# Kernel optimization log

Measured on AMD Instinct MI355X. Metric: run time of the kernel, lower is better.

Reference implementation:

```python
import jax, jax.numpy as jnp
import numpy as np
import math

HEADS = 16
HEAD_DIM = 64
MODEL_DIM = HEADS * HEAD_DIM
SEQ = 2048
BATCH = 2


def setup_inputs() -> dict:
    key = jax.random.key(0)
    ks = jax.random.split(key, 11)
    s = 0.02
    return {
        "query": jax.random.normal(ks[0], (SEQ, BATCH, MODEL_DIM), jnp.float32),
        "key": jax.random.normal(ks[1], (SEQ, BATCH, MODEL_DIM), jnp.float32),
        "value": jax.random.normal(ks[2], (SEQ, BATCH, MODEL_DIM), jnp.float32),
        "mask": jnp.ones((1, SEQ, 1), jnp.int32),
        "Wq": jax.random.normal(ks[3], (MODEL_DIM, MODEL_DIM), jnp.float32) * s,
        "bq": jax.random.normal(ks[4], (MODEL_DIM,), jnp.float32) * s,
        "Wk": jax.random.normal(ks[5], (MODEL_DIM, MODEL_DIM), jnp.float32) * s,
        "bk": jax.random.normal(ks[6], (MODEL_DIM,), jnp.float32) * s,
        "Wv": jax.random.normal(ks[7], (MODEL_DIM, MODEL_DIM), jnp.float32) * s,
        "bv": jax.random.normal(ks[8], (MODEL_DIM,), jnp.float32) * s,
        "Wo": jax.random.normal(ks[9], (MODEL_DIM, MODEL_DIM), jnp.float32) * s,
        "bo": jax.random.normal(ks[10], (MODEL_DIM,), jnp.float32) * s,
    }


def _proj(x, W, b):
    # torch nn.Linear: y = x @ W.T + b ; then view to [.., H, D]
    y = jnp.einsum("sbm,nm->sbn", x, W) + b
    return y.reshape(x.shape[0], x.shape[1], HEADS, HEAD_DIM)


def reference(query, key, value, mask, Wq, bq, Wk, bk, Wv, bv, Wo, bo):
    # NOTE: original module applies mask to `score` AFTER softmax has been
    # taken, and the masked score is discarded -> mask has no effect.
    del mask
    seq_len, batch_size, _ = query.shape
    scale = 1.0 / math.sqrt(HEAD_DIM)
    q = _proj(query, Wq, bq)   # [S,B,H,D]
    k = _proj(key, Wk, bk)
    v = _proj(value, Wv, bv)
    score = jnp.einsum("ibhd,jbhd->ijbh", q, k) * scale  # [S,S,B,H]
    attn = jax.nn.softmax(score, axis=1)  # softmax over key axis j
    # dropout: eval-mode identity (deterministic baseline)
    x = jnp.einsum("ijbh,jbhd->ibhd", attn, v)
    x = x.reshape(seq_len, batch_size, MODEL_DIM)
    return jnp.einsum("sbm,nm->sbn", x, Wo) + bo
```

## Files before the change

kernel.cpp:

```cpp
#include <hip/hip_runtime.h>

#define SEQ    2048
#define NBATCH 2
#define NHEAD  16
#define HD     64
#define MD     1024
#define TOK    (SEQ * NBATCH)
#define WN8    (MD * MD / 8)

typedef __attribute__((ext_vector_type(4)))  float f32x4;
typedef __attribute__((ext_vector_type(16))) float f32x16;
typedef __attribute__((ext_vector_type(8)))  short bf16x8;
typedef __attribute__((ext_vector_type(8)))  unsigned short u16x8;

__device__ __forceinline__ unsigned short f2bf(float f) {
  union { float f; unsigned int u; } x; x.f = f;
  unsigned int u = x.u + 0x7fffu + ((x.u >> 16) & 1u);
  return (unsigned short)(u >> 16);
}

__device__ __forceinline__ unsigned cvtpk(float lo, float hi) {
  unsigned r;
  asm("v_cvt_pk_bf16_f32 %0, %1, %2" : "=v"(r) : "v"(lo), "v"(hi));
  return r;
}
__device__ __forceinline__ void plswap(unsigned &a, unsigned &b) {
  asm volatile("v_permlane32_swap_b32 %0, %1" : "+v"(a), "+v"(b));
}

__device__ __forceinline__ void gload_lds16(const void* g, void* l) {
  typedef const __attribute__((address_space(1))) unsigned int* gp_t;
  typedef __attribute__((address_space(3))) unsigned int* lp_t;
  __builtin_amdgcn_global_load_lds((gp_t)g, (lp_t)l, 16, 0, 0);
}

__global__ __launch_bounds__(256) void cvt_w(
    const float* __restrict__ wq, const float* __restrict__ wk,
    const float* __restrict__ wv, const float* __restrict__ wo,
    unsigned short* __restrict__ owq, unsigned short* __restrict__ owk,
    unsigned short* __restrict__ owv, unsigned short* __restrict__ owo) {
  const int i = blockIdx.x * 256 + threadIdx.x;
  const int s = i >> 17;
  const int r = i & (WN8 - 1);
  const float* src = s == 0 ? wq : (s == 1 ? wk : (s == 2 ? wv : wo));
  unsigned short* dst = s == 0 ? owq : (s == 1 ? owk : (s == 2 ? owv : owo));
  const float4* p = (const float4*)src + (size_t)r * 2;
  float4 a = p[0];
  float4 b = p[1];
  u16x8 o;
  o[0] = f2bf(a.x); o[1] = f2bf(a.y); o[2] = f2bf(a.z); o[3] = f2bf(a.w);
  o[4] = f2bf(b.x); o[5] = f2bf(b.y); o[6] = f2bf(b.z); o[7] = f2bf(b.w);
  *((u16x8*)dst + r) = o;
}

__global__ __launch_bounds__(512) void gemm_qkv(
    const float* __restrict__ Xq, const float* __restrict__ Xk,
    const float* __restrict__ Xv, const unsigned short* __restrict__ Wq,
    const unsigned short* __restrict__ Wk, const unsigned short* __restrict__ Wv,
    const float* __restrict__ bq, const float* __restrict__ bk, const float* __restrict__ bv,
    unsigned short* __restrict__ Qo, unsigned short* __restrict__ Ko,
    unsigned short* __restrict__ Vo, float qscale) {
  __shared__ unsigned short sA[3][128 * 32];
  __shared__ unsigned short sB[3][128 * 32];
  const int tid  = threadIdx.x;
  const int lane = tid & 63;
  const int wave = tid >> 6;
  const int wm   = (wave >> 2) << 6;
  const int wn   = (wave & 3) << 5;
  const int l15  = lane & 15;
  const int g    = lane >> 4;

  const int flat = blockIdx.x + (blockIdx.y << 3) + (blockIdx.z << 8);
  const int nx   = (flat & 63) >> 3;
  const int gr   = ((flat >> 6) << 3) + (flat & 7);
  const int ny   = gr & 31;
  const int z    = gr >> 5;

  const float* Xf; const unsigned short* Wb; const float* bias;
  if (z == 0)      { Xf = Xq; Wb = Wq; bias = bq; }
  else if (z == 1) { Xf = Xk; Wb = Wk; bias = bk; }
  else             { Xf = Xv; Wb = Wv; bias = bv; }
  int bM, bN;
  if (z < 2) { bM = ny << 7; bN = nx << 7; }
  else       { bM = nx << 7; bN = ny << 7; }
  const int bX = (z < 2) ? bM : bN;
  const int bW = (z < 2) ? bN : bM;
  unsigned short* sX3 = (z < 2) ? &sA[0][0] : &sB[0][0];
  unsigned short* sW3 = (z < 2) ? &sB[0][0] : &sA[0][0];

  f32x4 acc[4][2];
#pragma unroll
  for (int a_ = 0; a_ < 4; ++a_)
#pragma unroll
    for (int b_ = 0; b_ < 2; ++b_)
      acc[a_][b_] = f32x4{0.f, 0.f, 0.f, 0.f};

  const int r = tid >> 2, cc = tid & 3;
  const float* xsrc = Xf + (size_t)(bX + r) * MD + cc * 8;
  const unsigned short* wsrc = Wb + (size_t)(bW + r) * MD + cc * 8;

  float4 ra0, rb0, ra1, rb1;
  auto xissue0 = [&](int kt) {
    ra0 = *(const float4*)(xsrc + (kt << 5));
    rb0 = *(const float4*)(xsrc + (kt << 5) + 4);
  };
  auto xissue1 = [&](int kt) {
    ra1 = *(const float4*)(xsrc + (kt << 5));
    rb1 = *(const float4*)(xsrc + (kt << 5) + 4);
  };
  auto xwrite0 = [&](int c) {
    union { unsigned u[4]; bf16x8 v; } w;
    w.u[0] = cvtpk(ra0.x, ra0.y); w.u[1] = cvtpk(ra0.z, ra0.w);
    w.u[2] = cvtpk(rb0.x, rb0.y); w.u[3] = cvtpk(rb0.z, rb0.w);
    *(bf16x8*)(sX3 + c * 4096 + tid * 8) = w.v;
  };
  auto xwrite1 = [&](int c) {
    union { unsigned u[4]; bf16x8 v; } w;
    w.u[0] = cvtpk(ra1.x, ra1.y); w.u[1] = cvtpk(ra1.z, ra1.w);
    w.u[2] = cvtpk(rb1.x, rb1.y); w.u[3] = cvtpk(rb1.z, rb1.w);
    *(bf16x8*)(sX3 + c * 4096 + tid * 8) = w.v;
  };
  auto wissue = [&](int c, int kt) {
    gload_lds16(wsrc + (kt << 5), (char*)(sW3 + c * 4096) + tid * 16);
  };

  auto mfma_step = [&](int c) {
    bf16x8 af[4], bfr[2];
#pragma unroll
    for (int f = 0; f < 4; ++f)
      af[f] = *(const bf16x8*)&sA[c][(wm + f * 16 + l15) * 32 + g * 8];
#pragma unroll
    for (int f = 0; f < 2; ++f)
      bfr[f] = *(const bf16x8*)&sB[c][(wn + f * 16 + l15) * 32 + g * 8];
#pragma unroll
    for (int mf = 0; mf < 4; ++mf)
#pragma unroll
      for (int nf = 0; nf < 2; ++nf)
        acc[mf][nf] = __builtin_amdgcn_mfma_f32_16x16x32_bf16(af[mf], bfr[nf], acc[mf][nf], 0, 0, 0);
  };

  const int nk = MD >> 5;
  auto endwait = [&](int e) {
    if (e + 4 < nk)      asm volatile("s_waitcnt vmcnt(3)" ::: "memory");
    else if (e + 2 < nk) asm volatile("s_waitcnt vmcnt(1)" ::: "memory");
    else                 asm volatile("s_waitcnt vmcnt(0)" ::: "memory");
    asm volatile("s_waitcnt lgkmcnt(0)" ::: "memory");
    __builtin_amdgcn_s_barrier();
  };

  xissue0(0);
  xissue1(1);
  wissue(0, 0);
  wissue(1, 1);
  asm volatile("s_waitcnt vmcnt(4)" ::: "memory");
  xwrite0(0);
  asm volatile("s_waitcnt vmcnt(2)" ::: "memory");
  xwrite1(1);
  xissue0(2);
  xissue1(3);
  asm volatile("s_waitcnt vmcnt(4)" ::: "memory");
  asm volatile("s_waitcnt lgkmcnt(0)" ::: "memory");
  __builtin_amdgcn_s_barrier();

  for (int kt = 0; kt < nk; kt += 2) {
    if (kt + 2 < nk) { xwrite0((kt + 2) % 3); wissue((kt + 2) % 3, kt + 2); }
    if (kt + 4 < nk) xissue0(kt + 4);
    mfma_step(kt % 3);
    endwait(kt);
    if (kt + 3 < nk) { xwrite1((kt + 3) % 3); wissue((kt + 3) % 3, kt + 3); }
    if (kt + 5 < nk) xissue1(kt + 5);
    mfma_step((kt + 1) % 3);
    if (kt + 2 < nk) endwait(kt + 1);
  }

  if (z < 2) {
    unsigned short* O = (z == 0) ? Qo : Ko;
    const float scale = (z == 0) ? qscale : 1.0f;
#pragma unroll
    for (int nf = 0; nf < 2; ++nf) {
      const int cch = bN + wn + nf * 16 + l15;
      const float bb = bias[cch];
      const int h = cch >> 6, d = cch & 63;
#pragma unroll
      for (int mf = 0; mf < 4; ++mf)
#pragma unroll
        for (int i = 0; i < 4; ++i) {
          const int t = bM + wm + mf * 16 + (g << 2) + i;
          const int b = t & 1, s = t >> 1;
          O[((((b << 4) + h) * SEQ + s) << 6) + d] = f2bf((acc[mf][nf][i] + bb) * scale);
        }
    }
  } else {
#pragma unroll
    for (int mf = 0; mf < 4; ++mf)
#pragma unroll
      for (int i = 0; i < 4; ++i) {
        const int rch = bM + wm + mf * 16 + (g << 2) + i;
        const float bb = bias[rch];
        const int h = rch >> 6, d = rch & 63;
#pragma unroll
        for (int nf = 0; nf < 2; ++nf) {
          const int t = bN + wn + nf * 16 + l15;
          const int b = t & 1, s = t >> 1;
          Vo[((((b << 4) + h) << 6) + d) * SEQ + s] = f2bf(acc[mf][nf][i] + bb);
        }
      }
  }
}

__global__ __launch_bounds__(1024) void gemm_oproj(const unsigned short* __restrict__ A,
                                                   const unsigned short* __restrict__ B,
                                                   const float* __restrict__ bias,
                                                   float* __restrict__ O) {
  __shared__ unsigned short sA[3][128 * 32];
  __shared__ unsigned short sB[3][128 * 32];
  const int tid  = threadIdx.x;
  const int lane = tid & 63;
  const int wave = tid >> 6;
  const int wm   = (wave >> 2) << 5;
  const int wn   = (wave & 3) << 5;
  const int l15  = lane & 15;
  const int g    = lane >> 4;

  const int flat = blockIdx.x + (blockIdx.y << 3);
  const int nx   = (flat & 63) >> 3;
  const int gr   = ((flat >> 6) << 3) + (flat & 7);
  const int bM   = gr << 7;
  const int bN   = nx << 7;

  f32x4 acc[2][2];
#pragma unroll
  for (int a_ = 0; a_ < 2; ++a_)
#pragma unroll
    for (int b_ = 0; b_ < 2; ++b_)
      acc[a_][b_] = f32x4{0.f, 0.f, 0.f, 0.f};

  const int ct = tid & 511;
  const int r = ct >> 2, cc = ct & 3;
  const unsigned short* srow = (tid < 512)
      ? A + (size_t)(bM + r) * MD + cc * 8
      : B + (size_t)(bN + r) * MD + cc * 8;
  unsigned short* sdst3 = (tid < 512) ? &sA[0][0] : &sB[0][0];
  auto stage = [&](int c, int kt) {
    gload_lds16(srow + (kt << 5), (char*)(sdst3 + c * 4096) + ct * 16);
  };

  const int nk = MD >> 5;
  stage(0, 0);
  stage(1, 1);
  asm volatile("s_waitcnt vmcnt(1)" ::: "memory");
  __builtin_amdgcn_s_barrier();

  int cur = 0;
  for (int kt = 0; kt < nk; ++kt) {
    if (kt + 2 < nk) stage(cur == 0 ? 2 : cur - 1, kt + 2);
    bf16x8 af[2], bfr[2];
#pragma unroll
    for (int f = 0; f < 2; ++f)
      af[f] = *(const bf16x8*)&sA[cur][(wm + f * 16 + l15) * 32 + g * 8];
#pragma unroll
    for (int f = 0; f < 2; ++f)
      bfr[f] = *(const bf16x8*)&sB[cur][(wn + f * 16 + l15) * 32 + g * 8];
#pragma unroll
    for (int mf = 0; mf < 2; ++mf)
#pragma unroll
      for (int nf = 0; nf < 2; ++nf)
        acc[mf][nf] = __builtin_amdgcn_mfma_f32_16x16x32_bf16(af[mf], bfr[nf], acc[mf][nf], 0, 0, 0);
    if (kt + 2 < nk)
      asm volatile("s_waitcnt vmcnt(1)" ::: "memory");
    else if (kt + 1 < nk)
      asm volatile("s_waitcnt vmcnt(0)" ::: "memory");
    if (kt + 1 < nk) __builtin_amdgcn_s_barrier();
    cur = (cur == 2) ? 0 : cur + 1;
  }

#pragma unroll
  for (int nf = 0; nf < 2; ++nf) {
    const int cch = bN + wn + nf * 16 + l15;
    const float bb = bias[cch];
#pragma unroll
    for (int mf = 0; mf < 2; ++mf)
#pragma unroll
      for (int i = 0; i < 4; ++i) {
        const int t = bM + wm + mf * 16 + (g << 2) + i;
        O[(size_t)t * MD + cch] = acc[mf][nf][i] + bb;
      }
  }
}

__global__ __launch_bounds__(512) void attn_fwd(const unsigned short* __restrict__ Qg,
                                                const unsigned short* __restrict__ Kg,
                                                const unsigned short* __restrict__ Vg,
                                                unsigned short* __restrict__ Xout) {
  __shared__ __align__(16) char smem[65536];
  char* sKc = smem;
  char* sVc = smem + 32768;

  const int tid  = threadIdx.x;
  const int lane = tid & 63;
  const int wave = tid >> 6;
  const int ws   = wave & 3;
  const int grp  = wave >> 2;
  const int l31  = lane & 31;
  const int half = lane >> 5;
  const int bh   = blockIdx.y;
  const int q0w  = (blockIdx.x << 7) + (ws << 5);

  const unsigned short* Qb = Qg + (size_t)bh * (SEQ * HD);
  const char* Kb = (const char*)(Kg + (size_t)bh * (SEQ * HD));
  const char* Vb = (const char*)(Vg + (size_t)bh * (HD * SEQ));

  bf16x8 qf[4];
#pragma unroll
  for (int c = 0; c < 4; ++c)
    qf[c] = *(const bf16x8*)&Qb[(size_t)(q0w + l31) * HD + c * 16 + half * 8];

  f32x16 acc_o[2];
#pragma unroll
  for (int dt = 0; dt < 2; ++dt)
#pragma unroll
    for (int e = 0; e < 16; ++e) acc_o[dt][e] = 0.f;
  float lrow = 0.f;

  auto stage = [&](int c, int kt) {
#pragma unroll
    for (int h = 0; h < 2; ++h) {
      const int p = tid << 4;
      const int row = p >> 7;
      const int lcol = (p ^ ((row & 7) << 4)) & 127;
      const int kbase = (h << 10) + (kt << 6);
      gload_lds16(Kb + (size_t)(kbase + row) * (HD * 2) + lcol,
                  sKc + ((h * 2 + c) << 13) + p);
      gload_lds16(Vb + (size_t)row * (SEQ * 2) + (kbase << 1) + lcol,
                  sVc + ((h * 2 + c) << 13) + p);
    }
  };

  const char* myK = sKc + (grp << 14);
  const char* myV = sVc + (grp << 14);

  stage(0, 0);
  __syncthreads();
  int cur = 0;

  const int NT = SEQ / 2 / 64;
  for (int kt = 0; kt < NT; ++kt) {
    if (kt + 1 < NT) stage(cur ^ 1, kt + 1);

    f32x16 accs[2];
    __builtin_amdgcn_s_setprio(1);
#pragma unroll
    for (int ks = 0; ks < 2; ++ks) {
#pragma unroll
      for (int e = 0; e < 16; ++e) accs[ks][e] = 0.f;
      const int krow = ks * 32 + l31;
      const int swz  = (krow & 7) << 4;
#pragma unroll
      for (int c = 0; c < 4; ++c) {
        const int off = (krow << 7) + ((c * 32 + half * 16) ^ swz);
        bf16x8 kf = *(const bf16x8*)(myK + ((cur) << 13) + off);
        accs[ks] = __builtin_amdgcn_mfma_f32_32x32x16_bf16(kf, qf[c], accs[ks], 0, 0, 0);
      }
    }
    __builtin_amdgcn_s_setprio(0);

    float rsum = 0.f;
#pragma unroll
    for (int ks = 0; ks < 2; ++ks)
#pragma unroll
      for (int e = 0; e < 16; ++e) {
        const float pv = __builtin_amdgcn_exp2f(accs[ks][e]);
        accs[ks][e] = pv;
        rsum += pv;
      }
    lrow += rsum;

    bf16x8 pa[4];
#pragma unroll
    for (int ks = 0; ks < 2; ++ks)
#pragma unroll
      for (int hc = 0; hc < 2; ++hc) {
        const int b = hc * 8;
        unsigned X  = cvtpk(accs[ks][b + 0], accs[ks][b + 1]);
        unsigned X2 = cvtpk(accs[ks][b + 2], accs[ks][b + 3]);
        unsigned Y  = cvtpk(accs[ks][b + 4], accs[ks][b + 5]);
        unsigned Y2 = cvtpk(accs[ks][b + 6], accs[ks][b + 7]);
        plswap(X, Y);
        plswap(X2, Y2);
        union { unsigned u[4]; bf16x8 v; } w;
        w.u[0] = X; w.u[1] = X2; w.u[2] = Y; w.u[3] = Y2;
        pa[ks * 2 + hc] = w.v;
      }

    __builtin_amdgcn_s_setprio(1);
#pragma unroll
    for (int dt = 0; dt < 2; ++dt) {
      const int drow = dt * 32 + l31;
      const int swz  = (drow & 7) << 4;
#pragma unroll
      for (int kc = 0; kc < 4; ++kc) {
        const int off = (drow << 7) + ((kc * 32 + half * 16) ^ swz);
        bf16x8 vf = *(const bf16x8*)(myV + ((cur) << 13) + off);
        acc_o[dt] = __builtin_amdgcn_mfma_f32_32x32x16_bf16(vf, pa[kc], acc_o[dt], 0, 0, 0);
      }
    }
    __builtin_amdgcn_s_setprio(0);

    __syncthreads();
    cur ^= 1;
  }

  float lt = lrow + __shfl_xor(lrow, 32);
  float* dump  = (float*)smem;
  float* ldump = dump + 4 * 32 * 68;
  const int base = (ws * 32 + l31) * 68;

  if (grp == 1) {
#pragma unroll
    for (int dt = 0; dt < 2; ++dt)
#pragma unroll
      for (int r4 = 0; r4 < 4; ++r4) {
        const int d0 = dt * 32 + r4 * 8 + half * 4;
        const int e = r4 * 4;
        *(float2*)&dump[base + d0]     = float2{acc_o[dt][e + 0], acc_o[dt][e + 1]};
        *(float2*)&dump[base + d0 + 2] = float2{acc_o[dt][e + 2], acc_o[dt][e + 3]};
      }
    if (half == 0) ldump[ws * 32 + l31] = lt;
  }
  __syncthreads();
  if (grp == 0) {
    const float ltot = lt + ldump[ws * 32 + l31];
    const float inv = 1.f / ltot;
    const int b = bh >> 4, h = bh & 15;
    const int s = q0w + l31;
    const int t = s * NBATCH + b;
    unsigned short* Ot = Xout + (size_t)t * MD + (h << 6);
#pragma unroll
    for (int dt = 0; dt < 2; ++dt)
#pragma unroll
      for (int r4 = 0; r4 < 4; ++r4) {
        const int d0 = dt * 32 + r4 * 8 + half * 4;
        const int e = r4 * 4;
        float2 a0 = *(float2*)&dump[base + d0];
        float2 a1 = *(float2*)&dump[base + d0 + 2];
        uint2 w;
        w.x = cvtpk((acc_o[dt][e + 0] + a0.x) * inv, (acc_o[dt][e + 1] + a0.y) * inv);
        w.y = cvtpk((acc_o[dt][e + 2] + a1.x) * inv, (acc_o[dt][e + 3] + a1.y) * inv);
        *(uint2*)(Ot + d0) = w;
      }
  }
}

extern "C" void kernel_launch(void* const* d_in, const int* in_sizes, int n_in,
                              void* d_out, int out_size, void* d_ws, size_t ws_size,
                              hipStream_t stream) {
  const float* query = (const float*)d_in[0];
  const float* key   = (const float*)d_in[1];
  const float* value = (const float*)d_in[2];
  const float* Wq = (const float*)d_in[4];
  const float* bq = (const float*)d_in[5];
  const float* Wk = (const float*)d_in[6];
  const float* bk = (const float*)d_in[7];
  const float* Wv = (const float*)d_in[8];
  const float* bv = (const float*)d_in[9];
  const float* Wo = (const float*)d_in[10];
  const float* bo = (const float*)d_in[11];

  char* ws = (char*)d_ws;
  const size_t MB = 1024 * 1024;
  unsigned short* Xa  = (unsigned short*)(ws + 0 * MB);
  unsigned short* Wqb = (unsigned short*)(ws + 24 * MB);
  unsigned short* Wkb = (unsigned short*)(ws + 26 * MB);
  unsigned short* Wvb = (unsigned short*)(ws + 28 * MB);
  unsigned short* Wob = (unsigned short*)(ws + 30 * MB);
  unsigned short* Qb  = (unsigned short*)(ws + 32 * MB);
  unsigned short* Kb  = (unsigned short*)(ws + 40 * MB);
  unsigned short* Vb  = (unsigned short*)(ws + 48 * MB);

  cvt_w<<<4 * WN8 / 256, 256, 0, stream>>>(Wq, Wk, Wv, Wo, Wqb, Wkb, Wvb, Wob);

  const float kQScale = 0.125f * 1.44269504088896340736f;
  dim3 gQKV(MD / 128, TOK / 128, 3);
  gemm_qkv<<<gQKV, 512, 0, stream>>>(query, key, value, Wqb, Wkb, Wvb,
                                     bq, bk, bv, Qb, Kb, Vb, kQScale);

  dim3 gA(SEQ / 128, NBATCH * NHEAD);
  attn_fwd<<<gA, 512, 0, stream>>>(Qb, Kb, Vb, Xa);

  dim3 gO(MD / 128, TOK / 128);
  gemm_oproj<<<gO, 1024, 0, stream>>>(Xa, Wob, bo, (float*)d_out);
  (void)in_sizes; (void)n_in; (void)out_size; (void)ws_size;
}
```

Baseline: 107.9 us.

## Split QKV GEMM loads across 1024 threads with X and W wave groups

Doubles the QKV projection block to 1024 threads. The first 512 threads load and convert the fp32 activations and the other 512 issue the direct-to-LDS weight loads, so each half has its own wait counters. All 16 waves now do MFMA on a 32x32 sub-tile instead of 8 waves doing 64x32, which halves accumulators per thread and adds waves to hide latency. In exchange, each wave does less MFMA work per LDS fragment read, and barrier cost is spread over more waves.

```diff
diff --git a/kernel.cpp b/kernel.cpp
--- a/kernel.cpp
+++ b/kernel.cpp
@@ -53,7 +53,7 @@
   *((u16x8*)dst + r) = o;
 }
 
-__global__ __launch_bounds__(512) void gemm_qkv(
+__global__ __launch_bounds__(1024) void gemm_qkv(
     const float* __restrict__ Xq, const float* __restrict__ Xk,
     const float* __restrict__ Xv, const unsigned short* __restrict__ Wq,
     const unsigned short* __restrict__ Wk, const unsigned short* __restrict__ Wv,
@@ -65,10 +65,11 @@
   const int tid  = threadIdx.x;
   const int lane = tid & 63;
   const int wave = tid >> 6;
-  const int wm   = (wave >> 2) << 6;
+  const int wm   = (wave >> 2) << 5;
   const int wn   = (wave & 3) << 5;
   const int l15  = lane & 15;
   const int g    = lane >> 4;
+  const bool isX = tid < 512;
 
   const int flat = blockIdx.x + (blockIdx.y << 3) + (blockIdx.z << 8);
   const int nx   = (flat & 63) >> 3;
@@ -88,14 +89,15 @@
   unsigned short* sX3 = (z < 2) ? &sA[0][0] : &sB[0][0];
   unsigned short* sW3 = (z < 2) ? &sB[0][0] : &sA[0][0];
 
-  f32x4 acc[4][2];
-#pragma unroll
-  for (int a_ = 0; a_ < 4; ++a_)
+  f32x4 acc[2][2];
+#pragma unroll
+  for (int a_ = 0; a_ < 2; ++a_)
 #pragma unroll
     for (int b_ = 0; b_ < 2; ++b_)
       acc[a_][b_] = f32x4{0.f, 0.f, 0.f, 0.f};
 
-  const int r = tid >> 2, cc = tid & 3;
+  const int ct = tid & 511;
+  const int r = ct >> 2, cc = ct & 3;
   const float* xsrc = Xf + (size_t)(bX + r) * MD + cc * 8;
   const unsigned short* wsrc = Wb + (size_t)(bW + r) * MD + cc * 8;
 
@@ -112,28 +114,28 @@
     union { unsigned u[4]; bf16x8 v; } w;
     w.u[0] = cvtpk(ra0.x, ra0.y); w.u[1] = cvtpk(ra0.z, ra0.w);
     w.u[2] = cvtpk(rb0.x, rb0.y); w.u[3] = cvtpk(rb0.z, rb0.w);
-    *(bf16x8*)(sX3 + c * 4096 + tid * 8) = w.v;
+    *(bf16x8*)(sX3 + c * 4096 + ct * 8) = w.v;
   };
   auto xwrite1 = [&](int c) {
     union { unsigned u[4]; bf16x8 v; } w;
     w.u[0] = cvtpk(ra1.x, ra1.y); w.u[1] = cvtpk(ra1.z, ra1.w);
     w.u[2] = cvtpk(rb1.x, rb1.y); w.u[3] = cvtpk(rb1.z, rb1.w);
-    *(bf16x8*)(sX3 + c * 4096 + tid * 8) = w.v;
+    *(bf16x8*)(sX3 + c * 4096 + ct * 8) = w.v;
   };
   auto wissue = [&](int c, int kt) {
-    gload_lds16(wsrc + (kt << 5), (char*)(sW3 + c * 4096) + tid * 16);
+    gload_lds16(wsrc + (kt << 5), (char*)(sW3 + c * 4096) + ct * 16);
   };
 
   auto mfma_step = [&](int c) {
-    bf16x8 af[4], bfr[2];
-#pragma unroll
-    for (int f = 0; f < 4; ++f)
+    bf16x8 af[2], bfr[2];
+#pragma unroll
+    for (int f = 0; f < 2; ++f)
       af[f] = *(const bf16x8*)&sA[c][(wm + f * 16 + l15) * 32 + g * 8];
 #pragma unroll
     for (int f = 0; f < 2; ++f)
       bfr[f] = *(const bf16x8*)&sB[c][(wn + f * 16 + l15) * 32 + g * 8];
 #pragma unroll
-    for (int mf = 0; mf < 4; ++mf)
+    for (int mf = 0; mf < 2; ++mf)
 #pragma unroll
       for (int nf = 0; nf < 2; ++nf)
         acc[mf][nf] = __builtin_amdgcn_mfma_f32_16x16x32_bf16(af[mf], bfr[nf], acc[mf][nf], 0, 0, 0);
@@ -141,34 +143,49 @@
 
   const int nk = MD >> 5;
   auto endwait = [&](int e) {
-    if (e + 4 < nk)      asm volatile("s_waitcnt vmcnt(3)" ::: "memory");
-    else if (e + 2 < nk) asm volatile("s_waitcnt vmcnt(1)" ::: "memory");
-    else                 asm volatile("s_waitcnt vmcnt(0)" ::: "memory");
+    if (isX) {
+      if (e + 4 < nk) asm volatile("s_waitcnt vmcnt(2)" ::: "memory");
+      else            asm volatile("s_waitcnt vmcnt(0)" ::: "memory");
+      asm volatile("s_waitcnt lgkmcnt(0)" ::: "memory");
+    } else {
+      if (e + 2 < nk) asm volatile("s_waitcnt vmcnt(1)" ::: "memory");
+      else            asm volatile("s_waitcnt vmcnt(0)" ::: "memory");
+    }
+    __builtin_amdgcn_s_barrier();
+  };
+
+  if (isX) {
+    xissue0(0);
+    xissue1(1);
+    asm volatile("s_waitcnt vmcnt(2)" ::: "memory");
+    xwrite0(0);
+    asm volatile("s_waitcnt vmcnt(0)" ::: "memory");
+    xwrite1(1);
+    xissue0(2);
+    xissue1(3);
     asm volatile("s_waitcnt lgkmcnt(0)" ::: "memory");
-    __builtin_amdgcn_s_barrier();
-  };
-
-  xissue0(0);
-  xissue1(1);
-  wissue(0, 0);
-  wissue(1, 1);
-  asm volatile("s_waitcnt vmcnt(4)" ::: "memory");
-  xwrite0(0);
-  asm volatile("s_waitcnt vmcnt(2)" ::: "memory");
-  xwrite1(1);
-  xissue0(2);
-  xissue1(3);
-  asm volatile("s_waitcnt vmcnt(4)" ::: "memory");
-  asm volatile("s_waitcnt lgkmcnt(0)" ::: "memory");
+  } else {
+    wissue(0, 0);
+    wissue(1, 1);
+    asm volatile("s_waitcnt vmcnt(0)" ::: "memory");
+  }
   __builtin_amdgcn_s_barrier();
 
   for (int kt = 0; kt < nk; kt += 2) {
-    if (kt + 2 < nk) { xwrite0((kt + 2) % 3); wissue((kt + 2) % 3, kt + 2); }
-    if (kt + 4 < nk) xissue0(kt + 4);
+    if (isX) {
+      if (kt + 2 < nk) xwrite0((kt + 2) % 3);
+      if (kt + 4 < nk) xissue0(kt + 4);
+    } else {
+      if (kt + 2 < nk) wissue((kt + 2) % 3, kt + 2);
+    }
     mfma_step(kt % 3);
     endwait(kt);
-    if (kt + 3 < nk) { xwrite1((kt + 3) % 3); wissue((kt + 3) % 3, kt + 3); }
-    if (kt + 5 < nk) xissue1(kt + 5);
+    if (isX) {
+      if (kt + 3 < nk) xwrite1((kt + 3) % 3);
+      if (kt + 5 < nk) xissue1(kt + 5);
+    } else {
+      if (kt + 3 < nk) wissue((kt + 3) % 3, kt + 3);
+    }
     mfma_step((kt + 1) % 3);
     if (kt + 2 < nk) endwait(kt + 1);
   }
@@ -182,7 +199,7 @@
       const float bb = bias[cch];
       const int h = cch >> 6, d = cch & 63;
 #pragma unroll
-      for (int mf = 0; mf < 4; ++mf)
+      for (int mf = 0; mf < 2; ++mf)
 #pragma unroll
         for (int i = 0; i < 4; ++i) {
           const int t = bM + wm + mf * 16 + (g << 2) + i;
@@ -192,7 +209,7 @@
     }
   } else {
 #pragma unroll
-    for (int mf = 0; mf < 4; ++mf)
+    for (int mf = 0; mf < 2; ++mf)
 #pragma unroll
       for (int i = 0; i < 4; ++i) {
         const int rch = bM + wm + mf * 16 + (g << 2) + i;
@@ -481,8 +498,8 @@
 
   const float kQScale = 0.125f * 1.44269504088896340736f;
   dim3 gQKV(MD / 128, TOK / 128, 3);
-  gemm_qkv<<<gQKV, 512, 0, stream>>>(query, key, value, Wqb, Wkb, Wvb,
-                                     bq, bk, bv, Qb, Kb, Vb, kQScale);
+  gemm_qkv<<<gQKV, 1024, 0, stream>>>(query, key, value, Wqb, Wkb, Wvb,
+                                      bq, bk, bv, Qb, Kb, Vb, kQScale);
 
   dim3 gA(SEQ / 128, NBATCH * NHEAD);
   attn_fwd<<<gA, 512, 0, stream>>>(Qb, Kb, Vb, Xa);
```

New measurement: 111.9 us. 1.04x slower.

## Replace triple-buffered QKV GEMM pipeline with simple double buffering

Applied to the files above, without the earlier changes.

The QKV projection GEMM drops its three-stage LDS ring, which prefetched two K-tiles ahead, and uses a two-buffer scheme instead. Each iteration now loads only the next tile, converts X to bf16 into LDS after the MFMA step, then waits and synchronises with a barrier. This cuts shared memory per block from about 48KB to 32KB and simplifies the wait-count bookkeeping, which may help occupancy. In exchange, less global-load latency is hidden behind compute, and there is a full vmcnt(0) wait plus a barrier on every K step.

```diff
diff --git a/kernel.cpp b/kernel.cpp
--- a/kernel.cpp
+++ b/kernel.cpp
@@ -60,8 +60,8 @@
     const float* __restrict__ bq, const float* __restrict__ bk, const float* __restrict__ bv,
     unsigned short* __restrict__ Qo, unsigned short* __restrict__ Ko,
     unsigned short* __restrict__ Vo, float qscale) {
-  __shared__ unsigned short sA[3][128 * 32];
-  __shared__ unsigned short sB[3][128 * 32];
+  __shared__ unsigned short sA[2][128 * 32];
+  __shared__ unsigned short sB[2][128 * 32];
   const int tid  = threadIdx.x;
   const int lane = tid & 63;
   const int wave = tid >> 6;
@@ -85,8 +85,8 @@
   else       { bM = nx << 7; bN = ny << 7; }
   const int bX = (z < 2) ? bM : bN;
   const int bW = (z < 2) ? bN : bM;
-  unsigned short* sX3 = (z < 2) ? &sA[0][0] : &sB[0][0];
-  unsigned short* sW3 = (z < 2) ? &sB[0][0] : &sA[0][0];
+  unsigned short* sX2 = (z < 2) ? &sA[0][0] : &sB[0][0];
+  unsigned short* sW2 = (z < 2) ? &sB[0][0] : &sA[0][0];
 
   f32x4 acc[4][2];
 #pragma unroll
@@ -99,29 +99,19 @@
   const float* xsrc = Xf + (size_t)(bX + r) * MD + cc * 8;
   const unsigned short* wsrc = Wb + (size_t)(bW + r) * MD + cc * 8;
 
-  float4 ra0, rb0, ra1, rb1;
-  auto xissue0 = [&](int kt) {
-    ra0 = *(const float4*)(xsrc + (kt << 5));
-    rb0 = *(const float4*)(xsrc + (kt << 5) + 4);
-  };
-  auto xissue1 = [&](int kt) {
-    ra1 = *(const float4*)(xsrc + (kt << 5));
-    rb1 = *(const float4*)(xsrc + (kt << 5) + 4);
-  };
-  auto xwrite0 = [&](int c) {
+  float4 ra, rb;
+  auto xissue = [&](int kt) {
+    ra = *(const float4*)(xsrc + (kt << 5));
+    rb = *(const float4*)(xsrc + (kt << 5) + 4);
+  };
+  auto xwrite = [&](int c) {
     union { unsigned u[4]; bf16x8 v; } w;
-    w.u[0] = cvtpk(ra0.x, ra0.y); w.u[1] = cvtpk(ra0.z, ra0.w);
-    w.u[2] = cvtpk(rb0.x, rb0.y); w.u[3] = cvtpk(rb0.z, rb0.w);
-    *(bf16x8*)(sX3 + c * 4096 + tid * 8) = w.v;
-  };
-  auto xwrite1 = [&](int c) {
-    union { unsigned u[4]; bf16x8 v; } w;
-    w.u[0] = cvtpk(ra1.x, ra1.y); w.u[1] = cvtpk(ra1.z, ra1.w);
-    w.u[2] = cvtpk(rb1.x, rb1.y); w.u[3] = cvtpk(rb1.z, rb1.w);
-    *(bf16x8*)(sX3 + c * 4096 + tid * 8) = w.v;
+    w.u[0] = cvtpk(ra.x, ra.y); w.u[1] = cvtpk(ra.z, ra.w);
+    w.u[2] = cvtpk(rb.x, rb.y); w.u[3] = cvtpk(rb.z, rb.w);
+    *(bf16x8*)(sX2 + c * 4096 + tid * 8) = w.v;
   };
   auto wissue = [&](int c, int kt) {
-    gload_lds16(wsrc + (kt << 5), (char*)(sW3 + c * 4096) + tid * 16);
+    gload_lds16(wsrc + (kt << 5), (char*)(sW2 + c * 4096) + tid * 16);
   };
 
   auto mfma_step = [&](int c) {
@@ -140,37 +130,24 @@
   };
 
   const int nk = MD >> 5;
-  auto endwait = [&](int e) {
-    if (e + 4 < nk)      asm volatile("s_waitcnt vmcnt(3)" ::: "memory");
-    else if (e + 2 < nk) asm volatile("s_waitcnt vmcnt(1)" ::: "memory");
-    else                 asm volatile("s_waitcnt vmcnt(0)" ::: "memory");
-    asm volatile("s_waitcnt lgkmcnt(0)" ::: "memory");
-    __builtin_amdgcn_s_barrier();
-  };
-
-  xissue0(0);
-  xissue1(1);
+  xissue(0);
   wissue(0, 0);
-  wissue(1, 1);
-  asm volatile("s_waitcnt vmcnt(4)" ::: "memory");
-  xwrite0(0);
-  asm volatile("s_waitcnt vmcnt(2)" ::: "memory");
-  xwrite1(1);
-  xissue0(2);
-  xissue1(3);
-  asm volatile("s_waitcnt vmcnt(4)" ::: "memory");
+  asm volatile("s_waitcnt vmcnt(1)" ::: "memory");
+  xwrite(0);
+  asm volatile("s_waitcnt vmcnt(0)" ::: "memory");
   asm volatile("s_waitcnt lgkmcnt(0)" ::: "memory");
   __builtin_amdgcn_s_barrier();
 
-  for (int kt = 0; kt < nk; kt += 2) {
-    if (kt + 2 < nk) { xwrite0((kt + 2) % 3); wissue((kt + 2) % 3, kt + 2); }
-    if (kt + 4 < nk) xissue0(kt + 4);
-    mfma_step(kt % 3);
-    endwait(kt);
-    if (kt + 3 < nk) { xwrite1((kt + 3) % 3); wissue((kt + 3) % 3, kt + 3); }
-    if (kt + 5 < nk) xissue1(kt + 5);
-    mfma_step((kt + 1) % 3);
-    if (kt + 2 < nk) endwait(kt + 1);
+  for (int kt = 0; kt < nk; ++kt) {
+    if (kt + 1 < nk) { xissue(kt + 1); wissue((kt + 1) & 1, kt + 1); }
+    mfma_step(kt & 1);
+    if (kt + 1 < nk) {
+      asm volatile("s_waitcnt vmcnt(1)" ::: "memory");
+      xwrite((kt + 1) & 1);
+      asm volatile("s_waitcnt vmcnt(0)" ::: "memory");
+      asm volatile("s_waitcnt lgkmcnt(0)" ::: "memory");
+      __builtin_amdgcn_s_barrier();
+    }
   }
 
   if (z < 2) {
```

New measurement: 107.4 us. Within noise of the previous version (-0.4%).
